# Performance work log

Hardware: AMD Instinct MI355X
Metric: run time of the kernel (lower is better)

The kernel has to match this reference:

```python
import jax, jax.numpy as jnp
import numpy as np

N, E, IN_DIM, HID, HEADS, LAYERS, NTYPES, NGRAPH = 50000, 600000, 64, 128, 8, 3, 10, 500
C = HID // HEADS
NEG_SLOPE = 0.2
EPS = 1e-5


def setup_inputs() -> dict:
    key = jax.random.key(0)
    ks = jax.random.split(key, 24)
    inp = {
        "x": jax.random.normal(ks[0], (N, IN_DIM), jnp.float32),
        "edge_index": jax.random.randint(ks[1], (2, E), 0, N),
        "node_types": jax.random.randint(ks[2], (N,), 0, NTYPES),
        "batch": jnp.sort(jax.random.randint(ks[3], (N,), 0, NGRAPH)),
        # node embedding linear
        "emb_W": jax.random.normal(ks[4], (IN_DIM, HID), jnp.float32) / np.sqrt(IN_DIM),
        "emb_b": jnp.zeros((HID,), jnp.float32),
        "ntype_emb": jax.random.normal(ks[5], (NTYPES, HID), jnp.float32) * 0.02,
        # stacked GAT layer params
        "gat_W": jax.random.normal(ks[6], (LAYERS, HID, HID), jnp.float32) / np.sqrt(HID),
        "att_src": jax.random.normal(ks[7], (LAYERS, HEADS, C), jnp.float32) * 0.1,
        "att_dst": jax.random.normal(ks[8], (LAYERS, HEADS, C), jnp.float32) * 0.1,
        "gat_b": jnp.zeros((LAYERS, HID), jnp.float32),
        "ln_g": jnp.ones((LAYERS, HID), jnp.float32),
        "ln_b": jnp.zeros((LAYERS, HID), jnp.float32),
        # global attention MLP
        "ga_W1": jax.random.normal(ks[9], (HID, HID), jnp.float32) / np.sqrt(HID),
        "ga_b1": jnp.zeros((HID,), jnp.float32),
        "ga_W2": jax.random.normal(ks[10], (HID, 1), jnp.float32) / np.sqrt(HID),
        "ga_b2": jnp.zeros((1,), jnp.float32),
        # graph classifier head
        "cls_W1": jax.random.normal(ks[11], (HID, HID), jnp.float32) / np.sqrt(HID),
        "cls_b1": jnp.zeros((HID,), jnp.float32),
        "cls_W2": jax.random.normal(ks[12], (HID, 1), jnp.float32) / np.sqrt(HID),
        "cls_b2": jnp.zeros((1,), jnp.float32),
    }
    return inp


def _layer_norm(h, g, b):
    mu = jnp.mean(h, axis=-1, keepdims=True)
    var = jnp.mean(jnp.square(h - mu), axis=-1, keepdims=True)
    return (h - mu) * jax.lax.rsqrt(var + EPS) * g + b


def _gat_layer(h, src, dst, W, a_src, a_dst, bias):
    # h: [N, HID] -> per-head projection [N, H, C]
    hp = (h @ W).reshape(N, HEADS, C)
    alpha_s = jnp.sum(hp * a_src, axis=-1)  # [N, H]
    alpha_d = jnp.sum(hp * a_dst, axis=-1)  # [N, H]
    e = jax.nn.leaky_relu(alpha_s[src] + alpha_d[dst], NEG_SLOPE)  # [E', H]
    # segment softmax over incoming edges of each destination node
    m = jax.ops.segment_max(e, dst, num_segments=N)
    ex = jnp.exp(e - m[dst])
    s = jax.ops.segment_sum(ex, dst, num_segments=N)
    alpha = ex / s[dst]  # every node has a self-loop, so s > 0
    msg = hp[src] * alpha[:, :, None]  # [E', H, C]
    out = jax.ops.segment_sum(msg, dst, num_segments=N)  # [N, H, C]
    return out.reshape(N, HID) + bias


def reference(x, edge_index, node_types, batch, emb_W, emb_b, ntype_emb,
              gat_W, att_src, att_dst, gat_b, ln_g, ln_b,
              ga_W1, ga_b1, ga_W2, ga_b2, cls_W1, cls_b1, cls_W2, cls_b2):
    # self-loops (PyG GATConv add_self_loops=True)
    loop = jnp.arange(N)
    src = jnp.concatenate([edge_index[0], loop])
    dst = jnp.concatenate([edge_index[1], loop])

    h = x @ emb_W + emb_b
    h = h + ntype_emb[node_types]

    for l in range(LAYERS):
        h_prev = h
        h = _gat_layer(h, src, dst, gat_W[l], att_src[l], att_dst[l], gat_b[l])
        h = _layer_norm(h, ln_g[l], ln_b[l])
        h = jax.nn.relu(h + h_prev)

    # global attention pooling: softmax over all nodes (dim 0, as in source)
    scores = jnp.tanh(h @ ga_W1 + ga_b1) @ ga_W2 + ga_b2  # [N, 1]
    attw = jax.nn.softmax(scores, axis=0)
    h_graph = jnp.sum(h * attw, axis=0)  # [HID]

    # global mean pool per graph
    sums = jax.ops.segment_sum(h, batch, num_segments=NGRAPH)  # [G, HID]
    cnts = jax.ops.segment_sum(jnp.ones((N, 1), h.dtype), batch, num_segments=NGRAPH)
    mean_pool = sums / jnp.maximum(cnts, 1.0)

    hg = h_graph + mean_pool  # broadcast [HID] + [G, HID]

    # graph classifier head (features_batch=None path), squeeze(-1)
    out = jax.nn.relu(hg @ cls_W1 + cls_b1) @ cls_W2 + cls_b2
    return out.squeeze(-1)  # [G]
```

## Files before the change

### kernel.cpp

```cpp
#include <hip/hip_runtime.h>
#include <hip/hip_bf16.h>
#include <math.h>

#define HID 128
#define HEADS 8
#define INDIM 64

typedef _Float16 f16x8 __attribute__((ext_vector_type(8)));
typedef _Float16 f16x2 __attribute__((ext_vector_type(2)));
typedef float f32x4 __attribute__((ext_vector_type(4)));

__device__ __forceinline__ float fast_tanh(float x) {
    return 1.f - 2.f / (__expf(2.f * x) + 1.f);
}

#if defined(__has_builtin)
#if __has_builtin(__builtin_amdgcn_fdot2)
#define HAVE_FDOT2 1
#endif
#endif

__global__ void prologue_kernel(const int* __restrict__ ei, int* __restrict__ deg,
                                const float* __restrict__ emb_W, const float* __restrict__ gat_W,
                                const float* __restrict__ ga_W1, _Float16* __restrict__ wt_emb,
                                _Float16* __restrict__ wt_gat, _Float16* __restrict__ wt_ga1,
                                const int* __restrict__ batch, int* __restrict__ gstart,
                                float* __restrict__ hgZ,
                                int E, int EE, int N, int G) {
    int i = blockIdx.x * blockDim.x + threadIdx.x;
    if (i < EE) {
        int dst = (i < E) ? ei[E + i] : (i - E);
        atomicAdd(&deg[dst], 1);
    }
    if (i < 8192) {
        int k = i >> 7, n = i & 127;
        wt_emb[n * 64 + k] = (_Float16)emb_W[i];
    } else if (i < 8192 + 49152) {
        int j = i - 8192;
        int l = j >> 14, r = j & 16383;
        int k = r >> 7, n = r & 127;
        wt_gat[l * 16384 + n * 128 + k] = (_Float16)gat_W[j];
    } else if (i < 73728) {
        int j = i - 57344;
        int k = j >> 7, n = j & 127;
        wt_ga1[n * 128 + k] = (_Float16)ga_W1[j];
    } else if (i < 73728 + 129) {
        hgZ[i - 73728] = 0.f;
    }
    if (i >= 100000 && i - 100000 <= G) {
        int g = i - 100000;
        int lo = 0, hi = N;
        while (lo < hi) {
            int mid = (lo + hi) >> 1;
            if (batch[mid] < g) lo = mid + 1; else hi = mid;
        }
        gstart[g] = lo;
    }
}

__global__ __launch_bounds__(256) void emb_l0_kernel(
    const float* __restrict__ x, const _Float16* __restrict__ wt_emb,
    const float* __restrict__ emb_b, const float* __restrict__ nemb,
    const int* __restrict__ ntypes,
    _Float16* __restrict__ h16,
    const _Float16* __restrict__ wt_g0,
    const float* __restrict__ asrc, const float* __restrict__ adst,
    _Float16* __restrict__ hp_out, float* __restrict__ als_out, float* __restrict__ ald_out,
    int PB, const int* __restrict__ ei, const int* __restrict__ deg,
    int* __restrict__ rowptr, int* __restrict__ woff, int* __restrict__ esrc,
    int* __restrict__ ctr,
    int N, int E, int EE, int NB)
{
    __shared__ _Float16 w_lds[128 * 136];
    __shared__ _Float16 a_lds[64 * 136];
    int t = threadIdx.x;

    if ((int)blockIdx.x >= PB) {
        int b = (int)blockIdx.x - PB;
        int i = b * 256 + t;
        int v = (i < N) ? deg[i] : 0;
        int pe = 0;
        for (int j = t; j < (b << 8); j += 256) pe += deg[j];
#pragma unroll
        for (int m = 32; m >= 1; m >>= 1) pe += __shfl_xor(pe, m, 64);
        int* itmp  = (int*)a_lds;
        int* itmp2 = itmp + 256;
        itmp[t] = v;
        if ((t & 63) == 0) itmp2[t >> 6] = pe;
        __syncthreads();
#pragma unroll
        for (int off = 1; off < 256; off <<= 1) {
            int xx = (t >= off) ? itmp[t - off] : 0;
            __syncthreads();
            itmp[t] += xx;
            __syncthreads();
        }
        pe = itmp2[0] + itmp2[1] + itmp2[2] + itmp2[3];
        int excl = itmp[t] - v + pe;
        if (i < N) { rowptr[i] = excl; woff[i] = excl; }
        if (b == 0 && t == 0) rowptr[N] = EE;
        __threadfence();
        __syncthreads();
        if (t == 0) {
            atomicAdd(ctr, 1);
            while (atomicAdd(ctr, 0) < NB) __builtin_amdgcn_s_sleep(16);
        }
        __syncthreads();
        for (int e = b * 256 + t; e < EE; e += NB * 256) {
            int src, dst;
            if (e < E) { src = ei[e]; dst = ei[E + e]; } else { src = dst = e - E; }
            int slot = atomicAdd(&woff[dst], 1);
            esrc[slot] = src;
        }
        return;
    }

    for (int i = t; i < 128 * 8; i += 256) {
        int row = i >> 3, c8 = i & 7;
        *(f16x8*)&w_lds[row * 72 + 8 * c8] = *(const f16x8*)&wt_emb[(size_t)row * 64 + 8 * c8];
    }
    int n0 = blockIdx.x * 64;
    for (int i = t; i < 64 * 8; i += 256) {
        int row = i >> 3, c8 = i & 7;
        f16x8 v = {};
        int n = n0 + row;
        if (n < N) {
            const float4* ptr = (const float4*)&x[(size_t)n * 64 + 8 * c8];
            float4 a = ptr[0], b4 = ptr[1];
            v[0] = (_Float16)a.x; v[1] = (_Float16)a.y;
            v[2] = (_Float16)a.z; v[3] = (_Float16)a.w;
            v[4] = (_Float16)b4.x; v[5] = (_Float16)b4.y;
            v[6] = (_Float16)b4.z; v[7] = (_Float16)b4.w;
        }
        *(f16x8*)&a_lds[row * 72 + 8 * c8] = v;
    }
    __syncthreads();

    int lane = t & 63, wv = t >> 6;
    int l15 = lane & 15, quad = lane >> 4;

    f32x4 acc[8];
#pragma unroll
    for (int c = 0; c < 8; ++c) acc[c] = (f32x4){0.f, 0.f, 0.f, 0.f};
#pragma unroll
    for (int kk = 0; kk < 2; ++kk) {
        f16x8 af = *(const f16x8*)&a_lds[(wv * 16 + l15) * 72 + kk * 32 + quad * 8];
#pragma unroll
        for (int c = 0; c < 8; ++c) {
            f16x8 bf = *(const f16x8*)&w_lds[(c * 16 + l15) * 72 + kk * 32 + quad * 8];
            acc[c] = __builtin_amdgcn_mfma_f32_16x16x32_f16(af, bf, acc[c], 0, 0, 0);
        }
    }
    float bv[8];
#pragma unroll
    for (int c = 0; c < 8; ++c) bv[c] = emb_b[c * 16 + l15];
    __syncthreads();
#pragma unroll
    for (int r = 0; r < 4; ++r) {
        int n = n0 + wv * 16 + quad * 4 + r;
        int nt = (n < N) ? ntypes[n] : 0;
#pragma unroll
        for (int c = 0; c < 8; ++c)
            a_lds[(wv * 16 + quad * 4 + r) * 136 + c * 16 + l15] =
                (_Float16)(acc[c][r] + bv[c] + nemb[nt * HID + c * 16 + l15]);
    }
    for (int i = t; i < 128 * 16; i += 256) {
        int row = i >> 4, c8 = i & 15;
        *(f16x8*)&w_lds[row * 136 + 8 * c8] = *(const f16x8*)&wt_g0[(size_t)row * 128 + 8 * c8];
    }
    __syncthreads();
    for (int i = t; i < 64 * 16; i += 256) {
        int row = i >> 4, c8 = i & 15;
        int n = n0 + row;
        if (n < N) *(f16x8*)&h16[(size_t)n * HID + 8 * c8] = *(const f16x8*)&a_lds[row * 136 + 8 * c8];
    }
#pragma unroll
    for (int c = 0; c < 8; ++c) acc[c] = (f32x4){0.f, 0.f, 0.f, 0.f};
#pragma unroll
    for (int kk = 0; kk < 4; ++kk) {
        f16x8 af = *(const f16x8*)&a_lds[(wv * 16 + l15) * 136 + kk * 32 + quad * 8];
#pragma unroll
        for (int c = 0; c < 8; ++c) {
            f16x8 bf = *(const f16x8*)&w_lds[(c * 16 + l15) * 136 + kk * 32 + quad * 8];
            acc[c] = __builtin_amdgcn_mfma_f32_16x16x32_f16(af, bf, acc[c], 0, 0, 0);
        }
    }
    __syncthreads();
#pragma unroll
    for (int c = 0; c < 8; ++c)
#pragma unroll
        for (int r = 0; r < 4; ++r)
            a_lds[(wv * 16 + quad * 4 + r) * 136 + c * 16 + l15] = (_Float16)acc[c][r];
    __syncthreads();
    for (int i = t; i < 64 * 16; i += 256) {
        int row = i >> 4, c8 = i & 15;
        int n = n0 + row;
        if (n < N) *(f16x8*)&hp_out[(size_t)n * HID + 8 * c8] = *(const f16x8*)&a_lds[row * 136 + 8 * c8];
    }
    for (int task2 = t; task2 < 512; task2 += 256) {
        int row = task2 >> 3, hd = task2 & 7;
        int n = n0 + row;
        if (n >= N) continue;
        f16x8 v0 = *(const f16x8*)&a_lds[row * 136 + hd * 16];
        f16x8 v1 = *(const f16x8*)&a_lds[row * 136 + hd * 16 + 8];
        float va = 0.f, vd = 0.f;
#pragma unroll
        for (int j = 0; j < 8; ++j) {
            va += (float)v0[j] * asrc[hd * 16 + j] + (float)v1[j] * asrc[hd * 16 + 8 + j];
            vd += (float)v0[j] * adst[hd * 16 + j] + (float)v1[j] * adst[hd * 16 + 8 + j];
        }
        als_out[n * HEADS + hd] = va;
        ald_out[n * HEADS + hd] = vd;
    }
}

__global__ __launch_bounds__(256) void proj_kernel(
    int mode, const _Float16* __restrict__ A16, const _Float16* __restrict__ Wt,
    const float* __restrict__ asrc, const float* __restrict__ adst,
    _Float16* __restrict__ hp_out, float* __restrict__ als, float* __restrict__ ald,
    const float* __restrict__ b1, const float* __restrict__ w2, const float* __restrict__ b2,
    float* __restrict__ escore, int N)
{
    __shared__ _Float16 w_lds[128 * 136];
    __shared__ _Float16 a_lds[64 * 136];
    int t = threadIdx.x;

    for (int i = t; i < 128 * 16; i += 256) {
        int row = i >> 4, c8 = i & 15;
        *(f16x8*)&w_lds[row * 136 + 8 * c8] = *(const f16x8*)&Wt[(size_t)row * 128 + 8 * c8];
    }
    int n0 = blockIdx.x * 64;
    for (int i = t; i < 64 * 16; i += 256) {
        int row = i >> 4, c8 = i & 15;
        f16x8 v = {};
        if (n0 + row < N) v = *(const f16x8*)&A16[(size_t)(n0 + row) * HID + 8 * c8];
        *(f16x8*)&a_lds[row * 136 + 8 * c8] = v;
    }
    __syncthreads();

    int lane = t & 63, wv = t >> 6;
    int l15 = lane & 15, quad = lane >> 4;

    f32x4 acc[8];
#pragma unroll
    for (int c = 0; c < 8; ++c) acc[c] = (f32x4){0.f, 0.f, 0.f, 0.f};
#pragma unroll
    for (int kk = 0; kk < 4; ++kk) {
        f16x8 af = *(const f16x8*)&a_lds[(wv * 16 + l15) * 136 + kk * 32 + quad * 8];
#pragma unroll
        for (int c = 0; c < 8; ++c) {
            f16x8 bf = *(const f16x8*)&w_lds[(c * 16 + l15) * 136 + kk * 32 + quad * 8];
            acc[c] = __builtin_amdgcn_mfma_f32_16x16x32_f16(af, bf, acc[c], 0, 0, 0);
        }
    }

    if (mode == 1) {
        __syncthreads();
#pragma unroll
        for (int c = 0; c < 8; ++c)
#pragma unroll
            for (int r = 0; r < 4; ++r)
                a_lds[(wv * 16 + quad * 4 + r) * 136 + c * 16 + l15] = (_Float16)acc[c][r];
        __syncthreads();
        for (int i = t; i < 64 * 16; i += 256) {
            int row = i >> 4, c8 = i & 15;
            int n = n0 + row;
            if (n < N) *(f16x8*)&hp_out[(size_t)n * HID + 8 * c8] = *(const f16x8*)&a_lds[row * 136 + 8 * c8];
        }
        for (int task2 = t; task2 < 512; task2 += 256) {
            int row = task2 >> 3, hd = task2 & 7;
            int n = n0 + row;
            if (n >= N) continue;
            f16x8 v0 = *(const f16x8*)&a_lds[row * 136 + hd * 16];
            f16x8 v1 = *(const f16x8*)&a_lds[row * 136 + hd * 16 + 8];
            float va = 0.f, vd = 0.f;
#pragma unroll
            for (int j = 0; j < 8; ++j) {
                va += (float)v0[j] * asrc[hd * 16 + j] + (float)v1[j] * asrc[hd * 16 + 8 + j];
                vd += (float)v0[j] * adst[hd * 16 + j] + (float)v1[j] * adst[hd * 16 + 8 + j];
            }
            als[n * HEADS + hd] = va;
            ald[n * HEADS + hd] = vd;
        }
    } else {
        float b2v = b2[0];
        float treg[4] = {0.f, 0.f, 0.f, 0.f};
#pragma unroll
        for (int c = 0; c < 8; ++c) {
            float b1v = b1[c * 16 + l15];
            float w2v = w2[c * 16 + l15];
#pragma unroll
            for (int r = 0; r < 4; ++r)
                treg[r] += fast_tanh(acc[c][r] + b1v) * w2v;
        }
#pragma unroll
        for (int r = 0; r < 4; ++r) {
            float v = treg[r];
#pragma unroll
            for (int m = 8; m >= 1; m >>= 1) v += __shfl_xor(v, m, 64);
            if (l15 == 0) {
                int n = n0 + wv * 16 + quad * 4 + r;
                if (n < N) escore[n] = __expf(v + b2v);
            }
        }
    }
}

__global__ void gat_aggregate_kernel(const int* __restrict__ rowptr, const int* __restrict__ esrc,
                                     const float* __restrict__ als, const float* __restrict__ ald,
                                     const _Float16* __restrict__ hp16, const float* __restrict__ gb,
                                     const float* __restrict__ lg, const float* __restrict__ lb,
                                     _Float16* __restrict__ h16, int N) {
    int wave = threadIdx.x >> 6;
    int lane = threadIdx.x & 63;
    int n = blockIdx.x * 4 + wave;
    if (n >= N) return;
    int esub = lane >> 4;
    int cg = lane & 15;
    int hd = cg >> 1;
    float adv = ald[n * HEADS + hd];
    int row = rowptr[n], end = rowptr[n + 1];
    int last = end - 1;
    float acc[8] = {0.f, 0.f, 0.f, 0.f, 0.f, 0.f, 0.f, 0.f};
    float sw = 0.f;
    for (int base = row; base < end; base += 16) {
        int iA = base + esub;
        int iB = iA + 4, iC = iA + 8, iD = iA + 12;
        int cA = iA <= last ? iA : last;
        int cB = iB <= last ? iB : last;
        int cC = iC <= last ? iC : last;
        int cD = iD <= last ? iD : last;
        int sA = esrc[cA], sB = esrc[cB], sC = esrc[cC], sD = esrc[cD];
        f16x8 pA = *(const f16x8*)&hp16[(size_t)sA * HID + cg * 8];
        f16x8 pB = *(const f16x8*)&hp16[(size_t)sB * HID + cg * 8];
        f16x8 pC = *(const f16x8*)&hp16[(size_t)sC * HID + cg * 8];
        f16x8 pD = *(const f16x8*)&hp16[(size_t)sD * HID + cg * 8];
        float aA = als[sA * HEADS + hd];
        float aB = als[sB * HEADS + hd];
        float aC = als[sC * HEADS + hd];
        float aD = als[sD * HEADS + hd];
        float lA = aA + adv; lA = lA > 0.f ? lA : 0.2f * lA;
        float lB = aB + adv; lB = lB > 0.f ? lB : 0.2f * lB;
        float lC = aC + adv; lC = lC > 0.f ? lC : 0.2f * lC;
        float lD = aD + adv; lD = lD > 0.f ? lD : 0.2f * lD;
        float wA = __expf(lA) * ((iA < end) ? 1.f : 0.f);
        float wB = __expf(lB) * ((iB < end) ? 1.f : 0.f);
        float wC = __expf(lC) * ((iC < end) ? 1.f : 0.f);
        float wD = __expf(lD) * ((iD < end) ? 1.f : 0.f);
        sw += (wA + wB) + (wC + wD);
#ifdef HAVE_FDOT2
        f16x2 wAB; wAB[0] = (_Float16)wA; wAB[1] = (_Float16)wB;
        f16x2 wCD; wCD[0] = (_Float16)wC; wCD[1] = (_Float16)wD;
#pragma unroll
        for (int j = 0; j < 8; ++j) {
            f16x2 prAB; prAB[0] = pA[j]; prAB[1] = pB[j];
            f16x2 prCD; prCD[0] = pC[j]; prCD[1] = pD[j];
            acc[j] = __builtin_amdgcn_fdot2(prAB, wAB, acc[j], false);
            acc[j] = __builtin_amdgcn_fdot2(prCD, wCD, acc[j], false);
        }
#else
#pragma unroll
        for (int j = 0; j < 8; ++j)
            acc[j] += wA * (float)pA[j] + wB * (float)pB[j]
                    + wC * (float)pC[j] + wD * (float)pD[j];
#endif
    }
#pragma unroll
    for (int m = 16; m <= 32; m <<= 1) {
        sw += __shfl_xor(sw, m, 64);
#pragma unroll
        for (int j = 0; j < 8; ++j) acc[j] += __shfl_xor(acc[j], m, 64);
    }
    float inv_sw = 1.f / sw;
    float4 g0 = ((const float4*)(gb + cg * 8))[0];
    float4 g1 = ((const float4*)(gb + cg * 8))[1];
    float v[8];
    v[0] = acc[0] * inv_sw + g0.x; v[1] = acc[1] * inv_sw + g0.y;
    v[2] = acc[2] * inv_sw + g0.z; v[3] = acc[3] * inv_sw + g0.w;
    v[4] = acc[4] * inv_sw + g1.x; v[5] = acc[5] * inv_sw + g1.y;
    v[6] = acc[6] * inv_sw + g1.z; v[7] = acc[7] * inv_sw + g1.w;
    float s = 0.f;
#pragma unroll
    for (int j = 0; j < 8; ++j) s += v[j];
#pragma unroll
    for (int m = 32; m >= 1; m >>= 1) s += __shfl_xor(s, m, 64);
    float mu = s * (1.f / 512.f);
    float d[8], sq = 0.f;
#pragma unroll
    for (int j = 0; j < 8; ++j) { d[j] = v[j] - mu; sq += d[j] * d[j]; }
#pragma unroll
    for (int m = 32; m >= 1; m >>= 1) sq += __shfl_xor(sq, m, 64);
    float inv = rsqrtf(sq * (1.f / 512.f) + 1e-5f);
    float4 lg0 = ((const float4*)(lg + cg * 8))[0];
    float4 lg1 = ((const float4*)(lg + cg * 8))[1];
    float4 lb0 = ((const float4*)(lb + cg * 8))[0];
    float4 lb1 = ((const float4*)(lb + cg * 8))[1];
    float lgv[8] = {lg0.x, lg0.y, lg0.z, lg0.w, lg1.x, lg1.y, lg1.z, lg1.w};
    float lbv[8] = {lb0.x, lb0.y, lb0.z, lb0.w, lb1.x, lb1.y, lb1.z, lb1.w};
    f16x8 hold = *(const f16x8*)&h16[(size_t)n * HID + cg * 8];
    f16x8 hnew;
#pragma unroll
    for (int j = 0; j < 8; ++j) {
        float r = d[j] * inv * lgv[j] + lbv[j] + (float)hold[j];
        hnew[j] = (_Float16)(r > 0.f ? r : 0.f);
    }
    if (esub == 0) *(f16x8*)&h16[(size_t)n * HID + cg * 8] = hnew;
}

__global__ __launch_bounds__(256) void pool_head_kernel(
    const _Float16* __restrict__ h16, const float* __restrict__ escore,
    const int* __restrict__ gstart,
    const float* __restrict__ W1, const float* __restrict__ b1,
    const float* __restrict__ W2, const float* __restrict__ b2,
    float* __restrict__ hgZ, int* __restrict__ ctr2,
    float* __restrict__ out, int G)
{
    int g = blockIdx.x;
    int t = threadIdx.x;
    int c = t & 127, grp = t >> 7;
    int s = gstart[g], e = gstart[g + 1];
    float msum = 0.f, asum = 0.f, z = 0.f;
    for (int n = s + grp; n < e; n += 2) {
        float hv = (float)h16[(size_t)n * HID + c];
        float es = escore[n];
        msum += hv;
        asum += es * hv;
        if (c == 0) z += es;
    }
    __shared__ float sm[2][HID];
    __shared__ float sa[2][HID];
    __shared__ float szs[2];
    __shared__ float hr[HID];
    __shared__ float part[2];
    sm[grp][c] = msum;
    sa[grp][c] = asum;
    if (c == 0) szs[grp] = z;
    __syncthreads();
    if (t < HID) atomicAdd(&hgZ[t], sa[0][t] + sa[1][t]);
    else if (t == HID) atomicAdd(&hgZ[HID], szs[0] + szs[1]);
    __threadfence();
    __syncthreads();
    if (t == 0) {
        atomicAdd(ctr2, 1);
        while (atomicAdd(ctr2, 0) < G) __builtin_amdgcn_s_sleep(16);
    }
    __syncthreads();
    float cnt = (float)(e - s);
    cnt = cnt > 1.f ? cnt : 1.f;
    if (t < HID) {
        float Z = hgZ[HID];
        hr[t] = hgZ[t] / Z + (sm[0][t] + sm[1][t]) / cnt;
    }
    __syncthreads();
    if (t < HID) {
        float acc = b1[t];
#pragma unroll 8
        for (int k = 0; k < HID; ++k) acc += hr[k] * W1[k * HID + t];
        acc = acc > 0.f ? acc : 0.f;
        float v = acc * W2[t];
#pragma unroll
        for (int m = 32; m >= 1; m >>= 1) v += __shfl_xor(v, m, 64);
        if ((t & 63) == 0) part[t >> 6] = v;
    }
    __syncthreads();
    if (t == 0) out[g] = part[0] + part[1] + b2[0];
}

extern "C" void kernel_launch(void* const* d_in, const int* in_sizes, int n_in,
                              void* d_out, int out_size, void* d_ws, size_t ws_size,
                              hipStream_t stream) {
    const float* x        = (const float*)d_in[0];
    const int*   ei       = (const int*)d_in[1];
    const int*   ntypes   = (const int*)d_in[2];
    const int*   batch    = (const int*)d_in[3];
    const float* emb_W    = (const float*)d_in[4];
    const float* emb_b    = (const float*)d_in[5];
    const float* nemb     = (const float*)d_in[6];
    const float* gat_W    = (const float*)d_in[7];
    const float* att_src  = (const float*)d_in[8];
    const float* att_dst  = (const float*)d_in[9];
    const float* gat_b    = (const float*)d_in[10];
    const float* ln_g     = (const float*)d_in[11];
    const float* ln_b     = (const float*)d_in[12];
    const float* ga_W1    = (const float*)d_in[13];
    const float* ga_b1    = (const float*)d_in[14];
    const float* ga_W2    = (const float*)d_in[15];
    const float* ga_b2    = (const float*)d_in[16];
    const float* cls_W1   = (const float*)d_in[17];
    const float* cls_b1   = (const float*)d_in[18];
    const float* cls_W2   = (const float*)d_in[19];
    const float* cls_b2   = (const float*)d_in[20];
    float* out = (float*)d_out;

    const int N  = in_sizes[2];
    const int E  = in_sizes[1] / 2;
    const int EE = E + N;
    const int G  = out_size;
    const int NB = (N + 255) / 256;

    float* ws      = (float*)d_ws;
    float* als     = ws;
    float* ald     = als + (size_t)N * HEADS;
    float* escore  = ald + (size_t)N * HEADS;
    float* hgZ     = escore + N;
    _Float16* h16  = (_Float16*)(hgZ + 136);
    _Float16* hp16 = h16 + (size_t)N * HID;
    _Float16* wt_emb = hp16 + (size_t)N * HID;
    _Float16* wt_gat = wt_emb + 128 * 64;
    _Float16* wt_ga1 = wt_gat + 3 * 128 * 128;
    int*   rowptr  = (int*)(wt_ga1 + 128 * 128);
    int*   woff    = rowptr + (N + 1);
    int*   deg     = woff + N;
    int*   ctr     = deg + N;
    int*   ctr2    = ctr + 1;
    int*   esrc    = ctr2 + 1;
    int*   gstart  = esrc + EE;

    int P1TOT = EE;
    if (P1TOT < 100000 + G + 1) P1TOT = 100000 + G + 1;

    hipMemsetAsync(deg, 0, ((size_t)N + 2) * sizeof(int), stream);
    prologue_kernel<<<(P1TOT + 255) / 256, 256, 0, stream>>>(
        ei, deg, emb_W, gat_W, ga_W1, wt_emb, wt_gat, wt_ga1,
        batch, gstart, hgZ, E, EE, N, G);

    const int PB = (N + 63) / 64;

    emb_l0_kernel<<<PB + NB, 256, 0, stream>>>(
        x, wt_emb, emb_b, nemb, ntypes, h16,
        wt_gat, att_src, att_dst, hp16, als, ald,
        PB, ei, deg, rowptr, woff, esrc, ctr, N, E, EE, NB);

    gat_aggregate_kernel<<<(N + 3) / 4, 256, 0, stream>>>(
        rowptr, esrc, als, ald, hp16,
        gat_b, ln_g, ln_b, h16, N);

    for (int l = 1; l < 3; ++l) {
        proj_kernel<<<PB, 256, 0, stream>>>(
            1, h16, wt_gat + (size_t)l * HID * HID,
            att_src + l * HID, att_dst + l * HID,
            hp16, als, ald, nullptr, nullptr, nullptr, nullptr, N);
        gat_aggregate_kernel<<<(N + 3) / 4, 256, 0, stream>>>(
            rowptr, esrc, als, ald, hp16,
            gat_b + l * HID, ln_g + l * HID, ln_b + l * HID, h16, N);
    }

    proj_kernel<<<PB, 256, 0, stream>>>(
        2, h16, wt_ga1, nullptr, nullptr,
        nullptr, nullptr, nullptr,
        ga_b1, ga_W2, ga_b2, escore, N);

    pool_head_kernel<<<G, 256, 0, stream>>>(
        h16, escore, gstart, cls_W1, cls_b1, cls_W2, cls_b2,
        hgZ, ctr2, out, G);
}
```

Before: 484.5 us.

## Split pooling into two kernels and schedule CSR-build blocks first

The pooled head no longer uses an in-kernel grid-wide spin barrier. It becomes a pooling kernel that writes per-graph sums and counts, with 512 threads and four node groups, followed by a separate head kernel. In the embedding kernel the CSR-building blocks now take the low block indices, so they are dispatched first and their spin barrier waits less behind projection blocks. The change adds one launch and a small workspace for sums, and removes the risk of a spin deadlock when not all blocks are resident.

```diff
diff --git a/kernel.cpp b/kernel.cpp
--- a/kernel.cpp
+++ b/kernel.cpp
@@ -66,7 +66,7 @@
     const _Float16* __restrict__ wt_g0,
     const float* __restrict__ asrc, const float* __restrict__ adst,
     _Float16* __restrict__ hp_out, float* __restrict__ als_out, float* __restrict__ ald_out,
-    int PB, const int* __restrict__ ei, const int* __restrict__ deg,
+    const int* __restrict__ ei, const int* __restrict__ deg,
     int* __restrict__ rowptr, int* __restrict__ woff, int* __restrict__ esrc,
     int* __restrict__ ctr,
     int N, int E, int EE, int NB)
@@ -75,8 +75,8 @@
     __shared__ _Float16 a_lds[64 * 136];
     int t = threadIdx.x;
 
-    if ((int)blockIdx.x >= PB) {
-        int b = (int)blockIdx.x - PB;
+    if ((int)blockIdx.x < NB) {
+        int b = (int)blockIdx.x;
         int i = b * 256 + t;
         int v = (i < N) ? deg[i] : 0;
         int pe = 0;
@@ -119,7 +119,7 @@
         int row = i >> 3, c8 = i & 7;
         *(f16x8*)&w_lds[row * 72 + 8 * c8] = *(const f16x8*)&wt_emb[(size_t)row * 64 + 8 * c8];
     }
-    int n0 = blockIdx.x * 64;
+    int n0 = ((int)blockIdx.x - NB) * 64;
     for (int i = t; i < 64 * 8; i += 256) {
         int row = i >> 3, c8 = i & 7;
         f16x8 v = {};
@@ -407,61 +407,60 @@
     if (esub == 0) *(f16x8*)&h16[(size_t)n * HID + cg * 8] = hnew;
 }
 
-__global__ __launch_bounds__(256) void pool_head_kernel(
-    const _Float16* __restrict__ h16, const float* __restrict__ escore,
-    const int* __restrict__ gstart,
-    const float* __restrict__ W1, const float* __restrict__ b1,
-    const float* __restrict__ W2, const float* __restrict__ b2,
-    float* __restrict__ hgZ, int* __restrict__ ctr2,
-    float* __restrict__ out, int G)
-{
+__global__ void pool_graph_kernel(const _Float16* __restrict__ h16, const float* __restrict__ escore,
+                                  const int* __restrict__ gstart, float* __restrict__ sums,
+                                  float* __restrict__ cnts, float* __restrict__ hgZ, int G) {
     int g = blockIdx.x;
     int t = threadIdx.x;
     int c = t & 127, grp = t >> 7;
     int s = gstart[g], e = gstart[g + 1];
     float msum = 0.f, asum = 0.f, z = 0.f;
-    for (int n = s + grp; n < e; n += 2) {
+    for (int n = s + grp; n < e; n += 4) {
         float hv = (float)h16[(size_t)n * HID + c];
         float es = escore[n];
         msum += hv;
         asum += es * hv;
         if (c == 0) z += es;
     }
-    __shared__ float sm[2][HID];
-    __shared__ float sa[2][HID];
-    __shared__ float szs[2];
+    __shared__ float sm[4][HID];
+    __shared__ float sa[4][HID];
+    __shared__ float sz[4];
+    sm[grp][c] = msum;
+    sa[grp][c] = asum;
+    if (c == 0) sz[grp] = z;
+    __syncthreads();
+    if (t < HID) {
+        float m = sm[0][t] + sm[1][t] + sm[2][t] + sm[3][t];
+        float a = sa[0][t] + sa[1][t] + sa[2][t] + sa[3][t];
+        sums[(size_t)g * HID + t] = m;
+        atomicAdd(&hgZ[t], a);
+    } else if (t == HID) {
+        cnts[g] = (float)(e - s);
+        atomicAdd(&hgZ[HID], sz[0] + sz[1] + sz[2] + sz[3]);
+    }
+}
+
+__global__ void head_kernel(const float* __restrict__ hgZ, const float* __restrict__ sums,
+                            const float* __restrict__ cnts, const float* __restrict__ W1,
+                            const float* __restrict__ b1, const float* __restrict__ W2,
+                            const float* __restrict__ b2, float* __restrict__ out, int G) {
+    int g = blockIdx.x;
+    int t = threadIdx.x;
     __shared__ float hr[HID];
     __shared__ float part[2];
-    sm[grp][c] = msum;
-    sa[grp][c] = asum;
-    if (c == 0) szs[grp] = z;
-    __syncthreads();
-    if (t < HID) atomicAdd(&hgZ[t], sa[0][t] + sa[1][t]);
-    else if (t == HID) atomicAdd(&hgZ[HID], szs[0] + szs[1]);
-    __threadfence();
-    __syncthreads();
-    if (t == 0) {
-        atomicAdd(ctr2, 1);
-        while (atomicAdd(ctr2, 0) < G) __builtin_amdgcn_s_sleep(16);
-    }
-    __syncthreads();
-    float cnt = (float)(e - s);
+    float Z = hgZ[HID];
+    float cnt = cnts[g];
     cnt = cnt > 1.f ? cnt : 1.f;
-    if (t < HID) {
-        float Z = hgZ[HID];
-        hr[t] = hgZ[t] / Z + (sm[0][t] + sm[1][t]) / cnt;
-    }
-    __syncthreads();
-    if (t < HID) {
-        float acc = b1[t];
+    hr[t] = hgZ[t] / Z + sums[(size_t)g * HID + t] / cnt;
+    __syncthreads();
+    float acc = b1[t];
 #pragma unroll 8
-        for (int k = 0; k < HID; ++k) acc += hr[k] * W1[k * HID + t];
-        acc = acc > 0.f ? acc : 0.f;
-        float v = acc * W2[t];
-#pragma unroll
-        for (int m = 32; m >= 1; m >>= 1) v += __shfl_xor(v, m, 64);
-        if ((t & 63) == 0) part[t >> 6] = v;
-    }
+    for (int k = 0; k < HID; ++k) acc += hr[k] * W1[k * HID + t];
+    acc = acc > 0.f ? acc : 0.f;
+    float v = acc * W2[t];
+#pragma unroll
+    for (int m = 32; m >= 1; m >>= 1) v += __shfl_xor(v, m, 64);
+    if ((t & 63) == 0) part[t >> 6] = v;
     __syncthreads();
     if (t == 0) out[g] = part[0] + part[1] + b2[0];
 }
@@ -502,7 +501,9 @@
     float* als     = ws;
     float* ald     = als + (size_t)N * HEADS;
     float* escore  = ald + (size_t)N * HEADS;
-    float* hgZ     = escore + N;
+    float* sums    = escore + N;
+    float* cnts    = sums + (size_t)G * HID;
+    float* hgZ     = cnts + G;
     _Float16* h16  = (_Float16*)(hgZ + 136);
     _Float16* hp16 = h16 + (size_t)N * HID;
     _Float16* wt_emb = hp16 + (size_t)N * HID;
@@ -512,24 +513,23 @@
     int*   woff    = rowptr + (N + 1);
     int*   deg     = woff + N;
     int*   ctr     = deg + N;
-    int*   ctr2    = ctr + 1;
-    int*   esrc    = ctr2 + 1;
+    int*   esrc    = ctr + 1;
     int*   gstart  = esrc + EE;
 
     int P1TOT = EE;
     if (P1TOT < 100000 + G + 1) P1TOT = 100000 + G + 1;
 
-    hipMemsetAsync(deg, 0, ((size_t)N + 2) * sizeof(int), stream);
+    hipMemsetAsync(deg, 0, ((size_t)N + 1) * sizeof(int), stream);
     prologue_kernel<<<(P1TOT + 255) / 256, 256, 0, stream>>>(
         ei, deg, emb_W, gat_W, ga_W1, wt_emb, wt_gat, wt_ga1,
         batch, gstart, hgZ, E, EE, N, G);
 
     const int PB = (N + 63) / 64;
 
-    emb_l0_kernel<<<PB + NB, 256, 0, stream>>>(
+    emb_l0_kernel<<<NB + PB, 256, 0, stream>>>(
         x, wt_emb, emb_b, nemb, ntypes, h16,
         wt_gat, att_src, att_dst, hp16, als, ald,
-        PB, ei, deg, rowptr, woff, esrc, ctr, N, E, EE, NB);
+        ei, deg, rowptr, woff, esrc, ctr, N, E, EE, NB);
 
     gat_aggregate_kernel<<<(N + 3) / 4, 256, 0, stream>>>(
         rowptr, esrc, als, ald, hp16,
@@ -550,7 +550,6 @@
         nullptr, nullptr, nullptr,
         ga_b1, ga_W2, ga_b2, escore, N);
 
-    pool_head_kernel<<<G, 256, 0, stream>>>(
-        h16, escore, gstart, cls_W1, cls_b1, cls_W2, cls_b2,
-        hgZ, ctr2, out, G);
-}
+    pool_graph_kernel<<<G, 512, 0, stream>>>(h16, escore, gstart, sums, cnts, hgZ, G);
+    head_kernel<<<G, 128, 0, stream>>>(hgZ, sums, cnts, cls_W1, cls_b1, cls_W2, cls_b2, out, G);
+}
```

New measurement: 416.0 us. -14.1%, faster.
